# Optimization experiments

Hardware: AMD Instinct MI355X
Metric: run time of the kernel (lower is better)

## Reference

```python
import jax, jax.numpy as jnp
import numpy as np

# RetentionPolicy config (training branch, force_sample_probs=None, num_classes=None)
TRAIN_MIN_CLASSES = 20
TRAIN_MAX_CLASSES = 100
TRAIN_CLASS_THR = 0.5

BS, K = 16384, 8192


def setup_inputs() -> dict:
    key = jax.random.key(0)
    # shift logits down so the per-row count above the 0.5-prob threshold
    # varies and actually hits both the min and max clamps
    logits = jax.random.normal(key, (BS, K), dtype=jnp.float32) * 2.0 - 6.0
    return {"label_logits": logits}


def reference(label_logits):
    """Faithful jit-able translation of RetentionPolicy.forward (training mode).

    The torch version returns ragged (bs_idx, cls_idx) built by a python loop.
    Under jit we return the fixed-width padded equivalent:
      bs_idx, cls_idx: [bs, max_classes] int32, padded with -1
      mask:            [bs, max_classes] bool, True where valid.
    Flattening the valid entries reproduces torch.cat(bs_idx), torch.cat(cls_idx).
    """
    label_prob = jax.nn.sigmoid(label_logits)           # [bs, K]
    bs, k_total = label_prob.shape

    num_above_thr = jnp.sum(label_prob >= TRAIN_CLASS_THR, axis=1)        # [bs]
    num_train = jnp.clip(num_above_thr, TRAIN_MIN_CLASSES, TRAIN_MAX_CLASSES)

    # top max_classes probs per row, descending (== argsort desc then slice)
    _, top_idx = jax.lax.top_k(label_prob, TRAIN_MAX_CLASSES)             # [bs, max]

    mask = jnp.arange(TRAIN_MAX_CLASSES)[None, :] < num_train[:, None]    # [bs, max]

    # per-row ascending sort of the selected class indices (invalid -> K sorts last)
    cls_sorted = jnp.sort(jnp.where(mask, top_idx, k_total), axis=1)
    cls_idx = jnp.where(mask, cls_sorted, -1).astype(jnp.int32)
    bs_idx = jnp.where(mask, jnp.arange(bs, dtype=jnp.int32)[:, None], -1)

    return bs_idx, cls_idx, mask
```

## Files before the change

### kernel.cpp

```cpp
#include <hip/hip_runtime.h>
#include <stdint.h>


#define BSZ   16384
#define KDIM  8192
#define MAXC  100
#define TMIN  20
#define CAP   256

__device__ __forceinline__ uint32_t okey(float x) {
  uint32_t b = __float_as_uint(x);
  return (b & 0x80000000u) ? ~b : (b | 0x80000000u);
}

__global__ __launch_bounds__(256, 8)
void retention_kernel(const float* __restrict__ in,
                      int* __restrict__ out_bs,
                      int* __restrict__ out_cls,
                      int* __restrict__ out_mask) {
  const int tid  = threadIdx.x;
  const int row  = blockIdx.x;
  const int lane = tid & 63;

  __shared__ unsigned long long buf[CAP];
  __shared__ int sidx[128];
  __shared__ unsigned nb;

  const float4* src = (const float4*)(in + (size_t)row * KDIM);

  if (tid == 0) nb = 0u;
  __syncthreads();

  #pragma unroll
  for (int b = 0; b < 2; ++b) {
    float4 f[4];
    #pragma unroll
    for (int j = 0; j < 4; ++j) f[j] = src[tid + 256 * (4 * b + j)];
    #pragma unroll
    for (int j = 0; j < 4; ++j) {
      float v[4] = {f[j].x, f[j].y, f[j].z, f[j].w};
      #pragma unroll
      for (int m = 0; m < 4; ++m) {
        float x = v[m];
        bool q = (x >= -2.0f);
        unsigned long long mk = __ballot(q);
        if (mk) {
          unsigned bw = 0;
          if (lane == 0) bw = atomicAdd(&nb, (unsigned)__popcll(mk));
          bw = (unsigned)__shfl((int)bw, 0, 64);
          if (q) {
            unsigned p = bw + (unsigned)__popcll(mk & ((1ull << lane) - 1ull));
            if (p < CAP) {
              int idx = 4 * tid + 1024 * (4 * b + j) + m;
              buf[p] = ((unsigned long long)okey(x) << 32) | (unsigned)idx;
            }
          }
        }
      }
    }
  }
  __syncthreads();

  if (tid >= 64) return;
  int M = (int)nb;
  int T = -1;

  if (M < TMIN || M > CAP) {
    const float* rp = in + (size_t)row * KDIM;
    int cp = 0;
    for (int e = lane; e < KDIM; e += 64) cp += (rp[e] >= 0.0f);
    #pragma unroll
    for (int off = 32; off; off >>= 1) cp += __shfl_down(cp, off, 64);
    cp = __shfl(cp, 0, 64);
    T = min(max(cp, TMIN), MAXC);

    unsigned long long lo = 0, hi = 1ull << 45, t = 0;
    int c;
    while (true) {
      unsigned long long mid = lo + ((hi - lo) >> 1);
      c = 0;
      for (int e = lane; e < KDIM; e += 64) {
        unsigned long long comp =
            ((unsigned long long)okey(rp[e]) << 13) | (unsigned)(8191 - e);
        c += (comp > mid) ? 1 : 0;
      }
      #pragma unroll
      for (int off = 32; off; off >>= 1) c += __shfl_down(c, off, 64);
      c = __shfl(c, 0, 64);
      if (c >= T && c <= CAP) { t = mid; break; }
      if (c < T) hi = mid; else lo = mid;
    }
    unsigned base = 0;
    for (int e = lane; e < KDIM; e += 64) {
      unsigned long long comp =
          ((unsigned long long)okey(rp[e]) << 13) | (unsigned)(8191 - e);
      bool q = comp > t;
      unsigned long long mk = __ballot(q);
      if (q) buf[base + (unsigned)__popcll(mk & ((1ull << lane) - 1ull))] =
                 ((unsigned long long)okey(rp[e]) << 32) | (unsigned)e;
      base += (unsigned)__popcll(mk);
    }
    M = c;
    __threadfence_block();
  }

  uint32_t val[4]; int ix[4];
  #pragma unroll
  for (int r = 0; r < 4; ++r) {
    int s = r * 64 + lane;
    unsigned long long c = (s < M) ? buf[s] : 0x0000000000007FFFull;
    val[r] = (uint32_t)(c >> 32);
    ix[r]  = (int)(c & 0xFFFFFFFFull);
  }

  if (T < 0) {
    int cp = 0;
    #pragma unroll
    for (int r = 0; r < 4; ++r)
      cp += (int)__popcll(__ballot((val[r] & 0x80000000u) != 0u));
    T = min(max(cp, TMIN), MAXC);
  }

  uint32_t blo = 0, bhi = 0xFFFFFFFFu;
  while (blo < bhi) {
    uint32_t mid = blo + ((bhi - blo) >> 1);
    int c = 0;
    #pragma unroll
    for (int r = 0; r < 4; ++r) c += (int)__popcll(__ballot(val[r] > mid));
    if (c < T) bhi = mid; else blo = mid + 1;
  }
  const uint32_t vT = blo;
  int c_gt = 0, c_eq = 0;
  #pragma unroll
  for (int r = 0; r < 4; ++r) {
    c_gt += (int)__popcll(__ballot(val[r] > vT));
    c_eq += (int)__popcll(__ballot(val[r] == vT));
  }
  const int need = T - c_gt;
  int dcut = 0x3FFF;
  if (c_eq != need) {
    int lo2 = 0, hi2 = 0x7FFF;
    while (lo2 < hi2) {
      int mid = (lo2 + hi2) >> 1;
      int g = 0;
      #pragma unroll
      for (int r = 0; r < 4; ++r)
        g += (int)__popcll(__ballot(val[r] == vT && ix[r] <= mid));
      if (g >= need) hi2 = mid; else lo2 = mid + 1;
    }
    dcut = lo2;
  }

  unsigned base = 0;
  #pragma unroll
  for (int r = 0; r < 4; ++r) {
    bool sel = (val[r] > vT) || (val[r] == vT && ix[r] <= dcut);
    unsigned long long mk = __ballot(sel);
    if (sel) sidx[base + (unsigned)__popcll(mk & ((1ull << lane) - 1ull))] = ix[r];
    base += (unsigned)__popcll(mk);
  }
  __threadfence_block();

  int a0 = (lane < T)      ? sidx[lane]      : 0x7FFFFFFF;
  int a1 = (64 + lane < T) ? sidx[64 + lane] : 0x7FFFFFFF;
  #pragma unroll
  for (int k = 2; k <= 128; k <<= 1) {
    for (int j = k >> 1; j; j >>= 1) {
      if (j == 64) {
        int mn = min(a0, a1), mx = max(a0, a1);
        a0 = mn; a1 = mx;
      } else {
        int o0 = __shfl_xor(a0, j, 64);
        int o1 = __shfl_xor(a1, j, 64);
        const bool lower = (lane & j) == 0;
        const bool asc0 = ((lane & k) == 0);
        const bool asc1 = (((64 + lane) & k) == 0);
        a0 = (lower != asc0) ? max(a0, o0) : min(a0, o0);
        a1 = (lower != asc1) ? max(a1, o1) : min(a1, o1);
      }
    }
  }

  const size_t o = (size_t)row * MAXC;
  if (lane < MAXC) {
    const bool vv = lane < T;
    out_bs[o + lane]   = vv ? row : -1;
    out_cls[o + lane]  = vv ? a0 : -1;
    out_mask[o + lane] = vv ? 1 : 0;
  }
  const int p = 64 + lane;
  if (p < MAXC) {
    const bool vv = p < T;
    out_bs[o + p]   = vv ? row : -1;
    out_cls[o + p]  = vv ? a1 : -1;
    out_mask[o + p] = vv ? 1 : 0;
  }
}

extern "C" void kernel_launch(void* const* d_in, const int* in_sizes, int n_in,
                              void* d_out, int out_size, void* d_ws, size_t ws_size,
                              hipStream_t stream) {
  const float* logits = (const float*)d_in[0];
  int* out = (int*)d_out;
  int* out_bs   = out;
  int* out_cls  = out + (size_t)BSZ * MAXC;
  int* out_mask = out + 2 * (size_t)BSZ * MAXC;
  retention_kernel<<<BSZ, 256, 0, stream>>>(logits, out_bs, out_cls, out_mask);
}
```

Before: 692.4 us.

## Assign one wavefront per row, four rows per block, dropping block sync

The work split moves from one 256-thread block per row to one 64-lane wavefront per row, with four rows per block. Each wave compacts its candidates with a ballot-prefix running base instead of a shared atomic counter, and the block barriers are removed. Previously three of the four waves sat idle after the filter pass, so this should use the machine better and cut atomics and syncs. In exchange each wave must stream the full 32KB row by itself with more serial load iterations, and shared memory per block grows.

```diff
diff --git a/kernel.cpp b/kernel.cpp
--- a/kernel.cpp
+++ b/kernel.cpp
@@ -7,6 +7,7 @@
 #define MAXC  100
 #define TMIN  20
 #define CAP   256
+#define RPB   4
 
 __device__ __forceinline__ uint32_t okey(float x) {
   uint32_t b = __float_as_uint(x);
@@ -19,23 +20,23 @@
                       int* __restrict__ out_cls,
                       int* __restrict__ out_mask) {
   const int tid  = threadIdx.x;
-  const int row  = blockIdx.x;
+  const int wv   = tid >> 6;
   const int lane = tid & 63;
-
-  __shared__ unsigned long long buf[CAP];
-  __shared__ int sidx[128];
-  __shared__ unsigned nb;
+  const int row  = blockIdx.x * RPB + wv;
+
+  __shared__ unsigned long long buf_s[RPB][CAP];
+  __shared__ int sidx_s[RPB][128];
+  unsigned long long* buf = buf_s[wv];
+  int* sidx = sidx_s[wv];
 
   const float4* src = (const float4*)(in + (size_t)row * KDIM);
 
-  if (tid == 0) nb = 0u;
-  __syncthreads();
-
-  #pragma unroll
-  for (int b = 0; b < 2; ++b) {
+  unsigned base = 0;
+  #pragma unroll
+  for (int b = 0; b < 8; ++b) {
     float4 f[4];
     #pragma unroll
-    for (int j = 0; j < 4; ++j) f[j] = src[tid + 256 * (4 * b + j)];
+    for (int j = 0; j < 4; ++j) f[j] = src[lane + 64 * (4 * b + j)];
     #pragma unroll
     for (int j = 0; j < 4; ++j) {
       float v[4] = {f[j].x, f[j].y, f[j].z, f[j].w};
@@ -44,25 +45,20 @@
         float x = v[m];
         bool q = (x >= -2.0f);
         unsigned long long mk = __ballot(q);
-        if (mk) {
-          unsigned bw = 0;
-          if (lane == 0) bw = atomicAdd(&nb, (unsigned)__popcll(mk));
-          bw = (unsigned)__shfl((int)bw, 0, 64);
-          if (q) {
-            unsigned p = bw + (unsigned)__popcll(mk & ((1ull << lane) - 1ull));
-            if (p < CAP) {
-              int idx = 4 * tid + 1024 * (4 * b + j) + m;
-              buf[p] = ((unsigned long long)okey(x) << 32) | (unsigned)idx;
-            }
+        if (q) {
+          unsigned p = base + (unsigned)__popcll(mk & ((1ull << lane) - 1ull));
+          if (p < CAP) {
+            int idx = 4 * lane + 256 * (4 * b + j) + m;
+            buf[p] = ((unsigned long long)okey(x) << 32) | (unsigned)idx;
           }
         }
+        base += (unsigned)__popcll(mk);
       }
     }
   }
-  __syncthreads();
-
-  if (tid >= 64) return;
-  int M = (int)nb;
+  __threadfence_block();
+
+  int M = (int)base;
   int T = -1;
 
   if (M < TMIN || M > CAP) {
@@ -90,15 +86,15 @@
       if (c >= T && c <= CAP) { t = mid; break; }
       if (c < T) hi = mid; else lo = mid;
     }
-    unsigned base = 0;
+    unsigned fb = 0;
     for (int e = lane; e < KDIM; e += 64) {
       unsigned long long comp =
           ((unsigned long long)okey(rp[e]) << 13) | (unsigned)(8191 - e);
       bool q = comp > t;
       unsigned long long mk = __ballot(q);
-      if (q) buf[base + (unsigned)__popcll(mk & ((1ull << lane) - 1ull))] =
+      if (q) buf[fb + (unsigned)__popcll(mk & ((1ull << lane) - 1ull))] =
                  ((unsigned long long)okey(rp[e]) << 32) | (unsigned)e;
-      base += (unsigned)__popcll(mk);
+      fb += (unsigned)__popcll(mk);
     }
     M = c;
     __threadfence_block();
@@ -151,13 +147,13 @@
     dcut = lo2;
   }
 
-  unsigned base = 0;
+  unsigned sb = 0;
   #pragma unroll
   for (int r = 0; r < 4; ++r) {
     bool sel = (val[r] > vT) || (val[r] == vT && ix[r] <= dcut);
     unsigned long long mk = __ballot(sel);
-    if (sel) sidx[base + (unsigned)__popcll(mk & ((1ull << lane) - 1ull))] = ix[r];
-    base += (unsigned)__popcll(mk);
+    if (sel) sidx[sb + (unsigned)__popcll(mk & ((1ull << lane) - 1ull))] = ix[r];
+    sb += (unsigned)__popcll(mk);
   }
   __threadfence_block();
 
@@ -205,5 +201,5 @@
   int* out_bs   = out;
   int* out_cls  = out + (size_t)BSZ * MAXC;
   int* out_mask = out + 2 * (size_t)BSZ * MAXC;
-  retention_kernel<<<BSZ, 256, 0, stream>>>(logits, out_bs, out_cls, out_mask);
+  retention_kernel<<<BSZ / RPB, 256, 0, stream>>>(logits, out_bs, out_cls, out_mask);
 }
```

Result: no change. 682.8 us (-1.4%).
